# Kernel tuning notes

Measured on AMD Instinct MI355X. Metric: run time of the kernel, lower is better.

## Reference

```python
import jax, jax.numpy as jnp
import numpy as np

N_NODES = 100000
N_EDGES = 1600000
D = 128
NEG_SLOPE = 0.01  # torch F.leaky_relu default


def setup_inputs() -> dict:
    key = jax.random.key(0)
    k1, k2, k3, k4, k5 = jax.random.split(key, 5)
    nfeat = jax.random.normal(k1, (N_NODES, D), dtype=jnp.float32)
    edge_src = jax.random.randint(k2, (N_EDGES,), 0, N_NODES, dtype=jnp.int32)
    edge_dst = jax.random.randint(k3, (N_EDGES,), 0, N_NODES, dtype=jnp.int32)
    edge_w = jax.random.uniform(k4, (N_EDGES,), dtype=jnp.float32)
    W = jax.random.normal(k5, (D, D), dtype=jnp.float32) * (1.0 / np.sqrt(D))
    return {"nfeat": nfeat, "edge_src": edge_src, "edge_dst": edge_dst,
            "edge_w": edge_w, "W": W}


def reference(nfeat, edge_src, edge_dst, edge_w, W):
    # message: m_e = h[src_e] * w_e  (u_mul_e)
    msg = nfeat[edge_src] * edge_w[:, None]          # [E, D]
    # reduce: h_neighbor[v] = sum_{e: dst(e)=v} m_e  (fn.sum)
    h_neighbor = jax.ops.segment_sum(msg, edge_dst, num_segments=nfeat.shape[0])  # [N, D]
    # Bi-interaction residual: leaky_relu(Linear(h * h_neighbor)); dropout = identity (eval)
    out = jax.nn.leaky_relu((nfeat * h_neighbor) @ W.T, negative_slope=NEG_SLOPE)
    return out
```

## Files before the change

kernel.cpp:

```cpp
#include <hip/hip_runtime.h>
#include <hip/hip_fp16.h>

#define NNODES 100000
#define NEDGES 1600000
#define DIM    128
#define NEG_SLOPE 0.01f
#define NB_SCAN ((NNODES + 1023) / 1024)
#define NPART 8
#define PART_SZ ((NNODES + NPART - 1) / NPART)
#define PCAP 220000
#define PCUR_STRIDE 32
#define CHUNK 2048
#define GEMM_TILES ((NNODES + 63) / 64)

typedef _Float16     v8h __attribute__((ext_vector_type(8)));
typedef float        v4f __attribute__((ext_vector_type(4)));
typedef int          v4i __attribute__((ext_vector_type(4)));
typedef int          v2i __attribute__((ext_vector_type(2)));
typedef float        v4x __attribute__((ext_vector_type(4)));
typedef unsigned int v2u __attribute__((ext_vector_type(2)));
typedef unsigned int v4u __attribute__((ext_vector_type(4)));

static inline size_t align256(size_t x) { return (x + 255) & ~(size_t)255; }

union HU { unsigned int u; __half2 h; };

__global__ __launch_bounds__(256) void zero_f32(float* __restrict__ p, int n4) {
    int i = blockIdx.x * blockDim.x + threadIdx.x;
    int stride = gridDim.x * blockDim.x;
    float4 z = make_float4(0.f, 0.f, 0.f, 0.f);
    for (; i < n4; i += stride) ((float4*)p)[i] = z;
}

__global__ __launch_bounds__(256) void prep(const float* __restrict__ nf,
                                            __half* __restrict__ nf16,
                                            int* __restrict__ counts,
                                            int* __restrict__ pcur) {
    int i = blockIdx.x * 256 + threadIdx.x;
    int stride = gridDim.x * 256;
    for (int j = i; j < NNODES * DIM / 4; j += stride) {
        v4x v = __builtin_nontemporal_load((const v4x*)nf + j);
        HU a, b;
        a.h = __float22half2_rn(make_float2(v.x, v.y));
        b.h = __float22half2_rn(make_float2(v.z, v.w));
        ((uint2*)nf16)[j] = make_uint2(a.u, b.u);
    }
    v4i z = (v4i){0, 0, 0, 0};
    for (int j = i; j < NNODES / 4; j += stride)
        *((v4i*)counts + j) = z;
    if (i < NPART * PCUR_STRIDE) pcur[i] = 0;
}

__global__ __launch_bounds__(256) void split_edges(const int* __restrict__ esrc,
                                                   const int* __restrict__ edst,
                                                   const float* __restrict__ ew,
                                                   int* __restrict__ pcur,
                                                   int2* __restrict__ pairs) {
    __shared__ int wtot[4][NPART];
    __shared__ int wbase[4][NPART];
    __shared__ int gbase[NPART];
    int tid = threadIdx.x;
    int wave = tid >> 6, lane = tid & 63;
    unsigned long long lt = (1ull << lane) - 1ull;

    int nq = NEDGES / 4;
    int qA = (blockIdx.x * CHUNK >> 2) + tid;
    int qB = qA + 256;

    v4i dA = (v4i){0,0,0,0}, sA = (v4i){0,0,0,0};
    v4x wA = (v4x){0,0,0,0};
    v4i dB = (v4i){0,0,0,0}, sB = (v4i){0,0,0,0};
    v4x wB = (v4x){0,0,0,0};
    bool vA = qA < nq, vB = qB < nq;
    if (vA) {
        dA = __builtin_nontemporal_load((const v4i*)edst + qA);
        sA = __builtin_nontemporal_load((const v4i*)esrc + qA);
        wA = __builtin_nontemporal_load((const v4x*)ew + qA);
    }
    if (vB) {
        dB = __builtin_nontemporal_load((const v4i*)edst + qB);
        sB = __builtin_nontemporal_load((const v4i*)esrc + qB);
        wB = __builtin_nontemporal_load((const v4x*)ew + qB);
    }

    int prt[8]; int rnk[8]; int2 pv[8];
    #pragma unroll
    for (int k = 0; k < 4; ++k) {
        int d = dA[k], s = sA[k];
        int p = vA ? (int)((unsigned)d / PART_SZ) : -1;
        prt[k] = p;
        pv[k] = make_int2(((d - p * PART_SZ) << 17) | s, __float_as_int(wA[k]));
        int d2 = dB[k], s2 = sB[k];
        int p2 = vB ? (int)((unsigned)d2 / PART_SZ) : -1;
        prt[k + 4] = p2;
        pv[k + 4] = make_int2(((d2 - p2 * PART_SZ) << 17) | s2, __float_as_int(wB[k]));
    }

    int runcnt = 0;
    #pragma unroll
    for (int s = 0; s < 8; ++s) {
        int myp = prt[s];
        unsigned long long mymask = 0;
        int addc = 0;
        #pragma unroll
        for (int p = 0; p < NPART; ++p) {
            unsigned long long m = __ballot(myp == p);
            if (myp == p) mymask = m;
            if (lane == p) addc = (int)__popcll(m);
        }
        int wr = __shfl(runcnt, myp < 0 ? 0 : myp);
        rnk[s] = wr + (int)__popcll(mymask & lt);
        runcnt += addc;
    }

    if (lane < NPART) wtot[wave][lane] = runcnt;
    __syncthreads();
    if (tid < NPART) {
        int t0 = wtot[0][tid], t1 = wtot[1][tid], t2 = wtot[2][tid], t3 = wtot[3][tid];
        wbase[0][tid] = 0; wbase[1][tid] = t0;
        wbase[2][tid] = t0 + t1; wbase[3][tid] = t0 + t1 + t2;
        gbase[tid] = atomicAdd(&pcur[tid * PCUR_STRIDE], t0 + t1 + t2 + t3);
    }
    __syncthreads();

    #pragma unroll
    for (int s = 0; s < 8; ++s) {
        int p = prt[s];
        if (p >= 0) {
            int slot = gbase[p] + wbase[wave][p] + rnk[s];
            if (slot < PCAP)
                pairs[(size_t)p * PCAP + slot] = pv[s];
        }
    }
}

__global__ __launch_bounds__(256) void hist_part(const int2* __restrict__ pairs,
                                                 const int* __restrict__ pcur,
                                                 int* __restrict__ counts) {
    int part = blockIdx.x & (NPART - 1);
    int n = pcur[part * PCUR_STRIDE];
    if (n > PCAP) n = PCAP;
    const int2* base = pairs + (size_t)part * PCAP;
    int cbase = part * PART_SZ;
    int t = (blockIdx.x >> 3) * 256 + threadIdx.x;
    int stride = (gridDim.x >> 3) * 256;
    for (int i = t; i < n; i += stride) {
        int2 pr = base[i];
        atomicAdd(&counts[cbase + ((unsigned)pr.x >> 17)], 1);
    }
}

__global__ __launch_bounds__(256) void scan1(const int* __restrict__ counts,
                                             int* __restrict__ offsets,
                                             int* __restrict__ blocksum) {
    __shared__ int lds[256];
    int tid = threadIdx.x;
    int base = blockIdx.x * 1024 + tid * 4;
    int c0 = (base + 0 < NNODES) ? counts[base + 0] : 0;
    int c1 = (base + 1 < NNODES) ? counts[base + 1] : 0;
    int c2 = (base + 2 < NNODES) ? counts[base + 2] : 0;
    int c3 = (base + 3 < NNODES) ? counts[base + 3] : 0;
    int t = c0 + c1 + c2 + c3;
    lds[tid] = t;
    __syncthreads();
    for (int d = 1; d < 256; d <<= 1) {
        int v = lds[tid];
        int add = (tid >= d) ? lds[tid - d] : 0;
        __syncthreads();
        lds[tid] = v + add;
        __syncthreads();
    }
    int incl = lds[tid];
    int excl = incl - t;
    if (base + 0 < NNODES) offsets[base + 0] = excl;
    if (base + 1 < NNODES) offsets[base + 1] = excl + c0;
    if (base + 2 < NNODES) offsets[base + 2] = excl + c0 + c1;
    if (base + 3 < NNODES) offsets[base + 3] = excl + c0 + c1 + c2;
    if (tid == 255) blocksum[blockIdx.x] = incl;
}

__global__ __launch_bounds__(128) void scan2p(int* __restrict__ blocksum, int nb) {
    __shared__ int lds[128];
    int tid = threadIdx.x;
    int v = (tid < nb) ? blocksum[tid] : 0;
    lds[tid] = v;
    __syncthreads();
    for (int d = 1; d < 128; d <<= 1) {
        int x = lds[tid];
        int add = (tid >= d) ? lds[tid - d] : 0;
        __syncthreads();
        lds[tid] = x + add;
        __syncthreads();
    }
    if (tid < nb) blocksum[tid] = lds[tid] - v;
}

__global__ __launch_bounds__(256) void scan3(int* __restrict__ offsets,
                                             const int* __restrict__ blocksum,
                                             int* __restrict__ cursor) {
    int add = blocksum[blockIdx.x];
    int base = blockIdx.x * 1024 + threadIdx.x * 4;
    #pragma unroll
    for (int i = 0; i < 4; ++i) {
        int idx = base + i;
        if (idx < NNODES) { int o = offsets[idx] + add; offsets[idx] = o; cursor[idx] = o; }
    }
}

__global__ __launch_bounds__(256) void fill_part2(const int2* __restrict__ pairs,
                                                  const int* __restrict__ pcur,
                                                  int* __restrict__ cursor,
                                                  int2* __restrict__ bins) {
    int part = blockIdx.x & (NPART - 1);
    int n = pcur[part * PCUR_STRIDE];
    if (n > PCAP) n = PCAP;
    const int2* base = pairs + (size_t)part * PCAP;
    int cbase = part * PART_SZ;
    int t = (blockIdx.x >> 3) * 256 + threadIdx.x;
    int stride = (gridDim.x >> 3) * 256;
    for (int i = t; i < n; i += stride) {
        int2 pr = base[i];
        int d = cbase + ((unsigned)pr.x >> 17);
        int p = atomicAdd(&cursor[d], 1);
        bins[p] = make_int2(pr.x & 0x1FFFF, pr.y);
    }
}

__global__ __launch_bounds__(256) void pull_x16(const __half* __restrict__ nf16,
                                                const int* __restrict__ offsets,
                                                const int* __restrict__ counts,
                                                const int2* __restrict__ bins,
                                                __half* __restrict__ x16) {
    int gid = blockIdx.x * 256 + threadIdx.x;
    int v = gid >> 5;
    int lane = gid & 31;
    if (v >= NNODES) return;
    int start = offsets[v];
    int end = start + counts[v];
    const uint2* nf2 = (const uint2*)nf16;
    float4 a0 = make_float4(0.f, 0.f, 0.f, 0.f);
    float4 a1 = make_float4(0.f, 0.f, 0.f, 0.f);
    float4 a2 = make_float4(0.f, 0.f, 0.f, 0.f);
    float4 a3 = make_float4(0.f, 0.f, 0.f, 0.f);
    int k = start;
    for (; k + 4 <= end; k += 4) {
        v2i e0 = __builtin_nontemporal_load((const v2i*)bins + k);
        v2i e1 = __builtin_nontemporal_load((const v2i*)bins + k + 1);
        v2i e2 = __builtin_nontemporal_load((const v2i*)bins + k + 2);
        v2i e3 = __builtin_nontemporal_load((const v2i*)bins + k + 3);
        uint2 u0 = nf2[(size_t)e0.x * 32 + lane];
        uint2 u1 = nf2[(size_t)e1.x * 32 + lane];
        uint2 u2 = nf2[(size_t)e2.x * 32 + lane];
        uint2 u3 = nf2[(size_t)e3.x * 32 + lane];
        float w0 = __int_as_float(e0.y), w1 = __int_as_float(e1.y);
        float w2 = __int_as_float(e2.y), w3 = __int_as_float(e3.y);
        HU h; float2 f;
        h.u = u0.x; f = __half22float2(h.h); a0.x += w0 * f.x; a0.y += w0 * f.y;
        h.u = u0.y; f = __half22float2(h.h); a0.z += w0 * f.x; a0.w += w0 * f.y;
        h.u = u1.x; f = __half22float2(h.h); a1.x += w1 * f.x; a1.y += w1 * f.y;
        h.u = u1.y; f = __half22float2(h.h); a1.z += w1 * f.x; a1.w += w1 * f.y;
        h.u = u2.x; f = __half22float2(h.h); a2.x += w2 * f.x; a2.y += w2 * f.y;
        h.u = u2.y; f = __half22float2(h.h); a2.z += w2 * f.x; a2.w += w2 * f.y;
        h.u = u3.x; f = __half22float2(h.h); a3.x += w3 * f.x; a3.y += w3 * f.y;
        h.u = u3.y; f = __half22float2(h.h); a3.z += w3 * f.x; a3.w += w3 * f.y;
    }
    for (; k < end; ++k) {
        v2i e = __builtin_nontemporal_load((const v2i*)bins + k);
        float w = __int_as_float(e.y);
        uint2 u = nf2[(size_t)e.x * 32 + lane];
        HU h; float2 f;
        h.u = u.x; f = __half22float2(h.h); a0.x += w * f.x; a0.y += w * f.y;
        h.u = u.y; f = __half22float2(h.h); a0.z += w * f.x; a0.w += w * f.y;
    }
    float4 acc;
    acc.x = (a0.x + a1.x) + (a2.x + a3.x);
    acc.y = (a0.y + a1.y) + (a2.y + a3.y);
    acc.z = (a0.z + a1.z) + (a2.z + a3.z);
    acc.w = (a0.w + a1.w) + (a2.w + a3.w);
    uint2 un = nf2[(size_t)v * 32 + lane];
    HU h; float2 f;
    h.u = un.x; f = __half22float2(h.h); acc.x *= f.x; acc.y *= f.y;
    h.u = un.y; f = __half22float2(h.h); acc.z *= f.x; acc.w *= f.y;
    HU o0, o1;
    o0.h = __float22half2_rn(make_float2(acc.x, acc.y));
    o1.h = __float22half2_rn(make_float2(acc.z, acc.w));
    v2u ov = (v2u){o0.u, o1.u};
    __builtin_nontemporal_store(ov, (v2u*)x16 + (size_t)v * 32 + lane);
}

__global__ __launch_bounds__(256) void gemm16(const __half* __restrict__ x16,
                                              const float* __restrict__ W,
                                              float* __restrict__ out) {
    __shared__ _Float16 Wl[128 * 128];
    __shared__ _Float16 Xl[64 * 128];
    int tid = threadIdx.x;

    const float4* Wg = (const float4*)W;
    for (int i = tid; i < 2048; i += 256) {
        int r = i >> 4, c = i & 15;
        float4 lo = Wg[(r * 128 + c * 8) >> 2];
        float4 hi = Wg[((r * 128 + c * 8) >> 2) + 1];
        v8h h;
        h[0] = (_Float16)lo.x; h[1] = (_Float16)lo.y; h[2] = (_Float16)lo.z; h[3] = (_Float16)lo.w;
        h[4] = (_Float16)hi.x; h[5] = (_Float16)hi.y; h[6] = (_Float16)hi.z; h[7] = (_Float16)hi.w;
        *(v8h*)&Wl[r * 128 + (c ^ (r & 7)) * 8] = h;
    }

    int rbase = blockIdx.x * 64;
    for (int i = tid; i < 1024; i += 256) {
        int r = i >> 4, c = i & 15;
        int grow = rbase + r;
        v4u u = (v4u){0u, 0u, 0u, 0u};
        if (grow < NNODES)
            u = __builtin_nontemporal_load((const v4u*)x16 + (size_t)grow * 16 + c);
        *(v4u*)&Xl[r * 128 + (c ^ (r & 7)) * 8] = u;
    }
    __syncthreads();

    int wave = tid >> 6;
    int lane = tid & 63;
    int n = lane & 15;
    int g = lane >> 4;

    v4f acc[8];
    #pragma unroll
    for (int jb = 0; jb < 8; ++jb) acc[jb] = (v4f){0.f, 0.f, 0.f, 0.f};

    #pragma unroll
    for (int kb = 0; kb < 4; ++kb) {
        v8h a = *(v8h*)&Xl[(wave * 16 + n) * 128 + (((kb * 4 + g) ^ (n & 7)) * 8)];
        #pragma unroll
        for (int jb = 0; jb < 8; ++jb) {
            v8h b = *(v8h*)&Wl[(jb * 16 + n) * 128 + (((kb * 4 + g) ^ (n & 7)) * 8)];
            acc[jb] = __builtin_amdgcn_mfma_f32_16x16x32_f16(a, b, acc[jb], 0, 0, 0);
        }
    }

    int row0 = rbase + wave * 16 + g * 4;
    #pragma unroll
    for (int jb = 0; jb < 8; ++jb) {
        #pragma unroll
        for (int reg = 0; reg < 4; ++reg) {
            int r = row0 + reg;
            if (r < NNODES) {
                float v = acc[jb][reg];
                v = v >= 0.f ? v : NEG_SLOPE * v;
                __builtin_nontemporal_store(v, out + (size_t)r * 128 + jb * 16 + n);
            }
        }
    }
}

__global__ __launch_bounds__(256) void hist_dst4(const int* __restrict__ edst,
                                                 int* __restrict__ counts) {
    int i = blockIdx.x * 256 + threadIdx.x;
    if (i < NEDGES / 4) {
        int4 d = ((const int4*)edst)[i];
        atomicAdd(&counts[d.x], 1);
        atomicAdd(&counts[d.y], 1);
        atomicAdd(&counts[d.z], 1);
        atomicAdd(&counts[d.w], 1);
    }
}

__global__ __launch_bounds__(256) void fill_part(const int* __restrict__ esrc,
                                                 const int* __restrict__ edst,
                                                 const float* __restrict__ ew,
                                                 int* __restrict__ cursor,
                                                 int2* __restrict__ bins) {
    int part = blockIdx.x & (NPART - 1);
    int lo = part * PART_SZ;
    int hi = lo + PART_SZ;
    int t = (blockIdx.x >> 3) * 256 + threadIdx.x;
    int stride = (gridDim.x >> 3) * 256;
    int nq = NEDGES / 4;
    for (int i = t; i < nq; i += stride) {
        int4 d = ((const int4*)edst)[i];
        int e = i * 4;
        if (d.x >= lo && d.x < hi) {
            int p = atomicAdd(&cursor[d.x], 1);
            bins[p] = make_int2(esrc[e + 0], __float_as_int(ew[e + 0]));
        }
        if (d.y >= lo && d.y < hi) {
            int p = atomicAdd(&cursor[d.y], 1);
            bins[p] = make_int2(esrc[e + 1], __float_as_int(ew[e + 1]));
        }
        if (d.z >= lo && d.z < hi) {
            int p = atomicAdd(&cursor[d.z], 1);
            bins[p] = make_int2(esrc[e + 2], __float_as_int(ew[e + 2]));
        }
        if (d.w >= lo && d.w < hi) {
            int p = atomicAdd(&cursor[d.w], 1);
            bins[p] = make_int2(esrc[e + 3], __float_as_int(ew[e + 3]));
        }
    }
}

__global__ __launch_bounds__(256) void scatter_edges(
    const float* __restrict__ nfeat, const int* __restrict__ esrc,
    const int* __restrict__ edst, const float* __restrict__ ew,
    float* __restrict__ hn) {
    long long t = (long long)blockIdx.x * 256 + threadIdx.x;
    int e = (int)(t >> 5);
    if (e >= NEDGES) return;
    int lane = (int)(t & 31);
    int s = esrc[e];
    int d = edst[e];
    float w = ew[e];
    float4 v = ((const float4*)(nfeat + (size_t)s * DIM))[lane];
    float* o = hn + (size_t)d * DIM + lane * 4;
    unsafeAtomicAdd(o + 0, v.x * w);
    unsafeAtomicAdd(o + 1, v.y * w);
    unsafeAtomicAdd(o + 2, v.z * w);
    unsafeAtomicAdd(o + 3, v.w * w);
}

__global__ __launch_bounds__(256) void elem_mul(const float* __restrict__ nfeat,
                                                float* __restrict__ hn, int n4) {
    int i = blockIdx.x * blockDim.x + threadIdx.x;
    int stride = gridDim.x * blockDim.x;
    for (; i < n4; i += stride) {
        float4 a = ((const float4*)nfeat)[i];
        float4 b = ((float4*)hn)[i];
        b.x *= a.x; b.y *= a.y; b.z *= a.z; b.w *= a.w;
        ((float4*)hn)[i] = b;
    }
}

__global__ __launch_bounds__(256) void bi_gemm2(
    const float* __restrict__ x, const float* __restrict__ W,
    float* __restrict__ out) {
    extern __shared__ float lds[];
    float4* W4  = (float4*)lds;
    float*  xs  = lds + 128 * 128;
    float4* xs4 = (float4*)xs;
    int tid = threadIdx.x;
    const float4* Wg = (const float4*)W;
    for (int i = tid; i < 128 * 32; i += 256) {
        int j = i >> 5, d4 = i & 31;
        W4[(j << 5) | (d4 ^ ((j >> 2) & 7))] = Wg[i];
    }
    __syncthreads();
    int tx = tid & 31, ty = tid >> 5;
    int j0 = tx << 2, r0 = ty << 2;
    int ntiles = NNODES / 32;
    for (int tile = blockIdx.x; tile < ntiles; tile += gridDim.x) {
        int rbase = tile * 32;
        for (int i = tid; i < 32 * 32; i += 256)
            xs4[i] = ((const float4*)x)[(size_t)rbase * 32 + i];
        __syncthreads();
        float acc[4][4];
        #pragma unroll
        for (int r = 0; r < 4; ++r)
            #pragma unroll
            for (int j = 0; j < 4; ++j) acc[r][j] = 0.f;
        #pragma unroll 4
        for (int d4 = 0; d4 < 32; ++d4) {
            float4 xv[4], wv[4];
            #pragma unroll
            for (int r = 0; r < 4; ++r) xv[r] = xs4[((r0 + r) << 5) | d4];
            #pragma unroll
            for (int j = 0; j < 4; ++j) {
                int jj = j0 + j;
                wv[j] = W4[(jj << 5) | (d4 ^ ((jj >> 2) & 7))];
            }
            #pragma unroll
            for (int r = 0; r < 4; ++r)
                #pragma unroll
                for (int j = 0; j < 4; ++j) {
                    acc[r][j] += xv[r].x * wv[j].x;
                    acc[r][j] += xv[r].y * wv[j].y;
                    acc[r][j] += xv[r].z * wv[j].z;
                    acc[r][j] += xv[r].w * wv[j].w;
                }
        }
        __syncthreads();
        #pragma unroll
        for (int r = 0; r < 4; ++r) {
            float4 o;
            o.x = acc[r][0] >= 0.f ? acc[r][0] : NEG_SLOPE * acc[r][0];
            o.y = acc[r][1] >= 0.f ? acc[r][1] : NEG_SLOPE * acc[r][1];
            o.z = acc[r][2] >= 0.f ? acc[r][2] : NEG_SLOPE * acc[r][2];
            o.w = acc[r][3] >= 0.f ? acc[r][3] : NEG_SLOPE * acc[r][3];
            size_t row = (size_t)(rbase + r0 + r);
            ((float4*)out)[row * (DIM / 4) + tx] = o;
        }
    }
}

extern "C" void kernel_launch(void* const* d_in, const int* in_sizes, int n_in,
                              void* d_out, int out_size, void* d_ws, size_t ws_size,
                              hipStream_t stream) {
    const float* nfeat = (const float*)d_in[0];
    const int*   esrc  = (const int*)d_in[1];
    const int*   edst  = (const int*)d_in[2];
    const float* ew    = (const float*)d_in[3];
    const float* W     = (const float*)d_in[4];
    float* out = (float*)d_out;

    size_t off = 0;
    size_t nf16_off = off;     off += align256((size_t)NNODES * DIM * 2);
    size_t x16_off = off;      off += align256((size_t)NNODES * DIM * 2);
    size_t cnt_off = off;      off += align256((size_t)NNODES * 4);
    size_t ofs_off = off;      off += align256((size_t)NNODES * 4);
    size_t cur_off = off;      off += align256((size_t)NNODES * 4);
    size_t pcur_off = off;     off += align256((size_t)NPART * PCUR_STRIDE * 4);
    size_t bsum_off = off;     off += align256((size_t)NB_SCAN * 4);
    size_t bins_off = off;     off += align256((size_t)NEDGES * 8);
    size_t need_mid = off;
    size_t pair_off = off;     off += align256((size_t)NPART * PCAP * 8);
    size_t need_full = off;

    char* ws = (char*)d_ws;

    if (ws_size >= need_mid) {
        __half* nf16 = (__half*)(ws + nf16_off);
        __half* x16  = (__half*)(ws + x16_off);
        int* counts = (int*)(ws + cnt_off);
        int* offsets = (int*)(ws + ofs_off);
        int* cursor = (int*)(ws + cur_off);
        int* pcur = (int*)(ws + pcur_off);
        int* blocksum = (int*)(ws + bsum_off);
        int2* bins = (int2*)(ws + bins_off);
        int2* pairs = (int2*)(ws + pair_off);

        prep<<<2048, 256, 0, stream>>>(nfeat, nf16, counts, pcur);
        if (ws_size >= need_full) {
            int sgrid = (NEDGES + CHUNK - 1) / CHUNK;
            split_edges<<<sgrid, 256, 0, stream>>>(esrc, edst, ew, pcur, pairs);
            hist_part<<<2048, 256, 0, stream>>>(pairs, pcur, counts);
            scan1<<<NB_SCAN, 256, 0, stream>>>(counts, offsets, blocksum);
            scan2p<<<1, 128, 0, stream>>>(blocksum, NB_SCAN);
            scan3<<<NB_SCAN, 256, 0, stream>>>(offsets, blocksum, cursor);
            fill_part2<<<2048, 256, 0, stream>>>(pairs, pcur, cursor, bins);
        } else {
            int e4grid = (NEDGES / 4 + 255) / 256;
            hist_dst4<<<e4grid, 256, 0, stream>>>(edst, counts);
            scan1<<<NB_SCAN, 256, 0, stream>>>(counts, offsets, blocksum);
            scan2p<<<1, 128, 0, stream>>>(blocksum, NB_SCAN);
            scan3<<<NB_SCAN, 256, 0, stream>>>(offsets, blocksum, cursor);
            fill_part<<<2048, 256, 0, stream>>>(esrc, edst, ew, cursor, bins);
        }
        int pgrid = (NNODES * 32 + 255) / 256;
        pull_x16<<<pgrid, 256, 0, stream>>>(nf16, offsets, counts, bins, x16);
        gemm16<<<GEMM_TILES, 256, 0, stream>>>(x16, W, out);
    } else {
        float* hn = (float*)ws;
        hipFuncSetAttribute((const void*)bi_gemm2,
                            hipFuncAttributeMaxDynamicSharedMemorySize, 81920);
        zero_f32<<<2048, 256, 0, stream>>>(hn, NNODES * DIM / 4);
        int sgrid = (NEDGES * 32 + 255) / 256;
        scatter_edges<<<sgrid, 256, 0, stream>>>(nfeat, esrc, edst, ew, hn);
        elem_mul<<<2048, 256, 0, stream>>>(nfeat, hn, NNODES * DIM / 4);
        bi_gemm2<<<512, 256, 81920, stream>>>(hn, W, out);
    }
}
```

Before: 274.6 us.

## Fuse neighbor pull into GEMM kernel with fp16 accumulation and prepacked W

```diff
diff --git a/kernel.cpp b/kernel.cpp
--- a/kernel.cpp
+++ b/kernel.cpp
@@ -18,12 +18,11 @@
 typedef int          v4i __attribute__((ext_vector_type(4)));
 typedef int          v2i __attribute__((ext_vector_type(2)));
 typedef float        v4x __attribute__((ext_vector_type(4)));
-typedef unsigned int v2u __attribute__((ext_vector_type(2)));
-typedef unsigned int v4u __attribute__((ext_vector_type(4)));
 
 static inline size_t align256(size_t x) { return (x + 255) & ~(size_t)255; }
 
 union HU { unsigned int u; __half2 h; };
+union U4H { uint4 u; __half2 h[4]; };
 
 __global__ __launch_bounds__(256) void zero_f32(float* __restrict__ p, int n4) {
     int i = blockIdx.x * blockDim.x + threadIdx.x;
@@ -33,7 +32,9 @@
 }
 
 __global__ __launch_bounds__(256) void prep(const float* __restrict__ nf,
+                                            const float* __restrict__ W,
                                             __half* __restrict__ nf16,
+                                            __half* __restrict__ W16,
                                             int* __restrict__ counts,
                                             int* __restrict__ pcur) {
     int i = blockIdx.x * 256 + threadIdx.x;
@@ -44,6 +45,16 @@
         a.h = __float22half2_rn(make_float2(v.x, v.y));
         b.h = __float22half2_rn(make_float2(v.z, v.w));
         ((uint2*)nf16)[j] = make_uint2(a.u, b.u);
+    }
+    const float4* Wg4 = (const float4*)W;
+    for (int j = i; j < DIM * DIM / 8; j += stride) {
+        float4 lo = Wg4[j * 2], hi = Wg4[j * 2 + 1];
+        HU a, b, c, d;
+        a.h = __float22half2_rn(make_float2(lo.x, lo.y));
+        b.h = __float22half2_rn(make_float2(lo.z, lo.w));
+        c.h = __float22half2_rn(make_float2(hi.x, hi.y));
+        d.h = __float22half2_rn(make_float2(hi.z, hi.w));
+        ((uint4*)W16)[j] = make_uint4(a.u, b.u, c.u, d.u);
     }
     v4i z = (v4i){0, 0, 0, 0};
     for (int j = i; j < NNODES / 4; j += stride)
@@ -144,8 +155,14 @@
     int cbase = part * PART_SZ;
     int t = (blockIdx.x >> 3) * 256 + threadIdx.x;
     int stride = (gridDim.x >> 3) * 256;
-    for (int i = t; i < n; i += stride) {
-        int2 pr = base[i];
+    int nh = n >> 1;
+    for (int i = t; i < nh; i += stride) {
+        v4i pr = __builtin_nontemporal_load((const v4i*)base + i);
+        atomicAdd(&counts[cbase + ((unsigned)pr.x >> 17)], 1);
+        atomicAdd(&counts[cbase + ((unsigned)pr.z >> 17)], 1);
+    }
+    if ((blockIdx.x >> 3) == 0 && threadIdx.x == 0 && (n & 1)) {
+        int2 pr = base[n - 1];
         atomicAdd(&counts[cbase + ((unsigned)pr.x >> 17)], 1);
     }
 }
@@ -196,20 +213,19 @@
 }
 
 __global__ __launch_bounds__(256) void scan3(int* __restrict__ offsets,
-                                             const int* __restrict__ blocksum,
-                                             int* __restrict__ cursor) {
+                                             const int* __restrict__ blocksum) {
     int add = blocksum[blockIdx.x];
     int base = blockIdx.x * 1024 + threadIdx.x * 4;
     #pragma unroll
     for (int i = 0; i < 4; ++i) {
         int idx = base + i;
-        if (idx < NNODES) { int o = offsets[idx] + add; offsets[idx] = o; cursor[idx] = o; }
+        if (idx < NNODES) offsets[idx] += add;
     }
 }
 
 __global__ __launch_bounds__(256) void fill_part2(const int2* __restrict__ pairs,
                                                   const int* __restrict__ pcur,
-                                                  int* __restrict__ cursor,
+                                                  int* __restrict__ offsets,
                                                   int2* __restrict__ bins) {
     int part = blockIdx.x & (NPART - 1);
     int n = pcur[part * PCUR_STRIDE];
@@ -218,102 +234,87 @@
     int cbase = part * PART_SZ;
     int t = (blockIdx.x >> 3) * 256 + threadIdx.x;
     int stride = (gridDim.x >> 3) * 256;
-    for (int i = t; i < n; i += stride) {
-        int2 pr = base[i];
+    int nh = n >> 1;
+    for (int i = t; i < nh; i += stride) {
+        v4i pr = __builtin_nontemporal_load((const v4i*)base + i);
+        int d0 = cbase + ((unsigned)pr.x >> 17);
+        int p0 = atomicAdd(&offsets[d0], 1);
+        bins[p0] = make_int2(pr.x & 0x1FFFF, pr.y);
+        int d1 = cbase + ((unsigned)pr.z >> 17);
+        int p1 = atomicAdd(&offsets[d1], 1);
+        bins[p1] = make_int2(pr.z & 0x1FFFF, pr.w);
+    }
+    if ((blockIdx.x >> 3) == 0 && threadIdx.x == 0 && (n & 1)) {
+        int2 pr = base[n - 1];
         int d = cbase + ((unsigned)pr.x >> 17);
-        int p = atomicAdd(&cursor[d], 1);
+        int p = atomicAdd(&offsets[d], 1);
         bins[p] = make_int2(pr.x & 0x1FFFF, pr.y);
     }
 }
 
-__global__ __launch_bounds__(256) void pull_x16(const __half* __restrict__ nf16,
-                                                const int* __restrict__ offsets,
-                                                const int* __restrict__ counts,
-                                                const int2* __restrict__ bins,
-                                                __half* __restrict__ x16) {
-    int gid = blockIdx.x * 256 + threadIdx.x;
-    int v = gid >> 5;
-    int lane = gid & 31;
-    if (v >= NNODES) return;
-    int start = offsets[v];
-    int end = start + counts[v];
-    const uint2* nf2 = (const uint2*)nf16;
-    float4 a0 = make_float4(0.f, 0.f, 0.f, 0.f);
-    float4 a1 = make_float4(0.f, 0.f, 0.f, 0.f);
-    float4 a2 = make_float4(0.f, 0.f, 0.f, 0.f);
-    float4 a3 = make_float4(0.f, 0.f, 0.f, 0.f);
-    int k = start;
-    for (; k + 4 <= end; k += 4) {
-        v2i e0 = __builtin_nontemporal_load((const v2i*)bins + k);
-        v2i e1 = __builtin_nontemporal_load((const v2i*)bins + k + 1);
-        v2i e2 = __builtin_nontemporal_load((const v2i*)bins + k + 2);
-        v2i e3 = __builtin_nontemporal_load((const v2i*)bins + k + 3);
-        uint2 u0 = nf2[(size_t)e0.x * 32 + lane];
-        uint2 u1 = nf2[(size_t)e1.x * 32 + lane];
-        uint2 u2 = nf2[(size_t)e2.x * 32 + lane];
-        uint2 u3 = nf2[(size_t)e3.x * 32 + lane];
-        float w0 = __int_as_float(e0.y), w1 = __int_as_float(e1.y);
-        float w2 = __int_as_float(e2.y), w3 = __int_as_float(e3.y);
-        HU h; float2 f;
-        h.u = u0.x; f = __half22float2(h.h); a0.x += w0 * f.x; a0.y += w0 * f.y;
-        h.u = u0.y; f = __half22float2(h.h); a0.z += w0 * f.x; a0.w += w0 * f.y;
-        h.u = u1.x; f = __half22float2(h.h); a1.x += w1 * f.x; a1.y += w1 * f.y;
-        h.u = u1.y; f = __half22float2(h.h); a1.z += w1 * f.x; a1.w += w1 * f.y;
-        h.u = u2.x; f = __half22float2(h.h); a2.x += w2 * f.x; a2.y += w2 * f.y;
-        h.u = u2.y; f = __half22float2(h.h); a2.z += w2 * f.x; a2.w += w2 * f.y;
-        h.u = u3.x; f = __half22float2(h.h); a3.x += w3 * f.x; a3.y += w3 * f.y;
-        h.u = u3.y; f = __half22float2(h.h); a3.z += w3 * f.x; a3.w += w3 * f.y;
-    }
-    for (; k < end; ++k) {
-        v2i e = __builtin_nontemporal_load((const v2i*)bins + k);
-        float w = __int_as_float(e.y);
-        uint2 u = nf2[(size_t)e.x * 32 + lane];
-        HU h; float2 f;
-        h.u = u.x; f = __half22float2(h.h); a0.x += w * f.x; a0.y += w * f.y;
-        h.u = u.y; f = __half22float2(h.h); a0.z += w * f.x; a0.w += w * f.y;
-    }
-    float4 acc;
-    acc.x = (a0.x + a1.x) + (a2.x + a3.x);
-    acc.y = (a0.y + a1.y) + (a2.y + a3.y);
-    acc.z = (a0.z + a1.z) + (a2.z + a3.z);
-    acc.w = (a0.w + a1.w) + (a2.w + a3.w);
-    uint2 un = nf2[(size_t)v * 32 + lane];
-    HU h; float2 f;
-    h.u = un.x; f = __half22float2(h.h); acc.x *= f.x; acc.y *= f.y;
-    h.u = un.y; f = __half22float2(h.h); acc.z *= f.x; acc.w *= f.y;
-    HU o0, o1;
-    o0.h = __float22half2_rn(make_float2(acc.x, acc.y));
-    o1.h = __float22half2_rn(make_float2(acc.z, acc.w));
-    v2u ov = (v2u){o0.u, o1.u};
-    __builtin_nontemporal_store(ov, (v2u*)x16 + (size_t)v * 32 + lane);
-}
-
-__global__ __launch_bounds__(256) void gemm16(const __half* __restrict__ x16,
-                                              const float* __restrict__ W,
-                                              float* __restrict__ out) {
-    __shared__ _Float16 Wl[128 * 128];
+__global__ __launch_bounds__(256) void pull_gemm(const __half* __restrict__ nf16,
+                                                 const __half* __restrict__ W16,
+                                                 const int* __restrict__ offsets,
+                                                 const int* __restrict__ counts,
+                                                 const int2* __restrict__ bins,
+                                                 float* __restrict__ out) {
     __shared__ _Float16 Xl[64 * 128];
     int tid = threadIdx.x;
-
-    const float4* Wg = (const float4*)W;
-    for (int i = tid; i < 2048; i += 256) {
-        int r = i >> 4, c = i & 15;
-        float4 lo = Wg[(r * 128 + c * 8) >> 2];
-        float4 hi = Wg[((r * 128 + c * 8) >> 2) + 1];
-        v8h h;
-        h[0] = (_Float16)lo.x; h[1] = (_Float16)lo.y; h[2] = (_Float16)lo.z; h[3] = (_Float16)lo.w;
-        h[4] = (_Float16)hi.x; h[5] = (_Float16)hi.y; h[6] = (_Float16)hi.z; h[7] = (_Float16)hi.w;
-        *(v8h*)&Wl[r * 128 + (c ^ (r & 7)) * 8] = h;
-    }
-
     int rbase = blockIdx.x * 64;
-    for (int i = tid; i < 1024; i += 256) {
-        int r = i >> 4, c = i & 15;
-        int grow = rbase + r;
-        v4u u = (v4u){0u, 0u, 0u, 0u};
-        if (grow < NNODES)
-            u = __builtin_nontemporal_load((const v4u*)x16 + (size_t)grow * 16 + c);
-        *(v4u*)&Xl[r * 128 + (c ^ (r & 7)) * 8] = u;
+    int gg = tid >> 4;
+    int l  = tid & 15;
+    const uint4* nfu4 = (const uint4*)nf16;
+
+    #pragma unroll
+    for (int t = 0; t < 4; ++t) {
+        int r = gg * 4 + t;
+        int v = rbase + r;
+        if (v < NNODES) {
+            int end = offsets[v];
+            int start = end - counts[v];
+            __half2 z2 = __float2half2_rn(0.f);
+            U4H a0, a1, a2, a3;
+            #pragma unroll
+            for (int j = 0; j < 4; ++j) { a0.h[j] = z2; a1.h[j] = z2; a2.h[j] = z2; a3.h[j] = z2; }
+            int k = start;
+            for (; k + 4 <= end; k += 4) {
+                v2i e0 = __builtin_nontemporal_load((const v2i*)bins + k);
+                v2i e1 = __builtin_nontemporal_load((const v2i*)bins + k + 1);
+                v2i e2 = __builtin_nontemporal_load((const v2i*)bins + k + 2);
+                v2i e3 = __builtin_nontemporal_load((const v2i*)bins + k + 3);
+                U4H u0, u1, u2, u3;
+                u0.u = nfu4[(size_t)e0.x * 16 + l];
+                u1.u = nfu4[(size_t)e1.x * 16 + l];
+                u2.u = nfu4[(size_t)e2.x * 16 + l];
+                u3.u = nfu4[(size_t)e3.x * 16 + l];
+                __half2 w0 = __float2half2_rn(__int_as_float(e0.y));
+                __half2 w1 = __float2half2_rn(__int_as_float(e1.y));
+                __half2 w2 = __float2half2_rn(__int_as_float(e2.y));
+                __half2 w3 = __float2half2_rn(__int_as_float(e3.y));
+                #pragma unroll
+                for (int j = 0; j < 4; ++j) {
+                    a0.h[j] = __hfma2(w0, u0.h[j], a0.h[j]);
+                    a1.h[j] = __hfma2(w1, u1.h[j], a1.h[j]);
+                    a2.h[j] = __hfma2(w2, u2.h[j], a2.h[j]);
+                    a3.h[j] = __hfma2(w3, u3.h[j], a3.h[j]);
+                }
+            }
+            for (; k < end; ++k) {
+                v2i e = __builtin_nontemporal_load((const v2i*)bins + k);
+                U4H u; u.u = nfu4[(size_t)e.x * 16 + l];
+                __half2 w = __float2half2_rn(__int_as_float(e.y));
+                #pragma unroll
+                for (int j = 0; j < 4; ++j) a0.h[j] = __hfma2(w, u.h[j], a0.h[j]);
+            }
+            U4H s, sf;
+            sf.u = nfu4[(size_t)v * 16 + l];
+            #pragma unroll
+            for (int j = 0; j < 4; ++j) {
+                __half2 t2 = __hadd2(__hadd2(a0.h[j], a1.h[j]), __hadd2(a2.h[j], a3.h[j]));
+                s.h[j] = __hmul2(t2, sf.h[j]);
+            }
+            *(uint4*)&Xl[r * 128 + ((l ^ (r & 7)) << 3)] = s.u;
+        }
     }
     __syncthreads();
 
@@ -321,6 +322,7 @@
     int lane = tid & 63;
     int n = lane & 15;
     int g = lane >> 4;
+    const v8h* w8 = (const v8h*)W16;
 
     v4f acc[8];
     #pragma unroll
@@ -328,10 +330,10 @@
 
     #pragma unroll
     for (int kb = 0; kb < 4; ++kb) {
-        v8h a = *(v8h*)&Xl[(wave * 16 + n) * 128 + (((kb * 4 + g) ^ (n & 7)) * 8)];
+        v8h a = *(v8h*)&Xl[(wave * 16 + n) * 128 + (((kb * 4 + g) ^ (n & 7)) << 3)];
         #pragma unroll
         for (int jb = 0; jb < 8; ++jb) {
-            v8h b = *(v8h*)&Wl[(jb * 16 + n) * 128 + (((kb * 4 + g) ^ (n & 7)) * 8)];
+            v8h b = w8[(jb * 16 + n) * 16 + kb * 4 + g];
             acc[jb] = __builtin_amdgcn_mfma_f32_16x16x32_f16(a, b, acc[jb], 0, 0, 0);
         }
     }
@@ -366,7 +368,7 @@
 __global__ __launch_bounds__(256) void fill_part(const int* __restrict__ esrc,
                                                  const int* __restrict__ edst,
                                                  const float* __restrict__ ew,
-                                                 int* __restrict__ cursor,
+                                                 int* __restrict__ offsets,
                                                  int2* __restrict__ bins) {
     int part = blockIdx.x & (NPART - 1);
     int lo = part * PART_SZ;
@@ -378,19 +380,19 @@
         int4 d = ((const int4*)edst)[i];
         int e = i * 4;
         if (d.x >= lo && d.x < hi) {
-            int p = atomicAdd(&cursor[d.x], 1);
+            int p = atomicAdd(&offsets[d.x], 1);
             bins[p] = make_int2(esrc[e + 0], __float_as_int(ew[e + 0]));
         }
         if (d.y >= lo && d.y < hi) {
-            int p = atomicAdd(&cursor[d.y], 1);
+            int p = atomicAdd(&offsets[d.y], 1);
             bins[p] = make_int2(esrc[e + 1], __float_as_int(ew[e + 1]));
         }
         if (d.z >= lo && d.z < hi) {
-            int p = atomicAdd(&cursor[d.z], 1);
+            int p = atomicAdd(&offsets[d.z], 1);
             bins[p] = make_int2(esrc[e + 2], __float_as_int(ew[e + 2]));
         }
         if (d.w >= lo && d.w < hi) {
-            int p = atomicAdd(&cursor[d.w], 1);
+            int p = atomicAdd(&offsets[d.w], 1);
             bins[p] = make_int2(esrc[e + 3], __float_as_int(ew[e + 3]));
         }
     }
@@ -500,10 +502,9 @@
 
     size_t off = 0;
     size_t nf16_off = off;     off += align256((size_t)NNODES * DIM * 2);
-    size_t x16_off = off;      off += align256((size_t)NNODES * DIM * 2);
+    size_t w16_off = off;      off += align256((size_t)DIM * DIM * 2);
     size_t cnt_off = off;      off += align256((size_t)NNODES * 4);
     size_t ofs_off = off;      off += align256((size_t)NNODES * 4);
-    size_t cur_off = off;      off += align256((size_t)NNODES * 4);
     size_t pcur_off = off;     off += align256((size_t)NPART * PCUR_STRIDE * 4);
     size_t bsum_off = off;     off += align256((size_t)NB_SCAN * 4);
     size_t bins_off = off;     off += align256((size_t)NEDGES * 8);
@@ -515,35 +516,32 @@
 
     if (ws_size >= need_mid) {
         __half* nf16 = (__half*)(ws + nf16_off);
-        __half* x16  = (__half*)(ws + x16_off);
+        __half* W16  = (__half*)(ws + w16_off);
         int* counts = (int*)(ws + cnt_off);
         int* offsets = (int*)(ws + ofs_off);
-        int* cursor = (int*)(ws + cur_off);
         int* pcur = (int*)(ws + pcur_off);
         int* blocksum = (int*)(ws + bsum_off);
         int2* bins = (int2*)(ws + bins_off);
         int2* pairs = (int2*)(ws + pair_off);
 
-        prep<<<2048, 256, 0, stream>>>(nfeat, nf16, counts, pcur);
+        prep<<<2048, 256, 0, stream>>>(nfeat, W, nf16, W16, counts, pcur);
         if (ws_size >= need_full) {
             int sgrid = (NEDGES + CHUNK - 1) / CHUNK;
             split_edges<<<sgrid, 256, 0, stream>>>(esrc, edst, ew, pcur, pairs);
             hist_part<<<2048, 256, 0, stream>>>(pairs, pcur, counts);
             scan1<<<NB_SCAN, 256, 0, stream>>>(counts, offsets, blocksum);
             scan2p<<<1, 128, 0, stream>>>(blocksum, NB_SCAN);
-            scan3<<<NB_SCAN, 256, 0, stream>>>(offsets, blocksum, cursor);
-            fill_part2<<<2048, 256, 0, stream>>>(pairs, pcur, cursor, bins);
+            scan3<<<NB_SCAN, 256, 0, stream>>>(offsets, blocksum);
+            fill_part2<<<2048, 256, 0, stream>>>(pairs, pcur, offsets, bins);
         } else {
             int e4grid = (NEDGES / 4 + 255) / 256;
             hist_dst4<<<e4grid, 256, 0, stream>>>(edst, counts);
             scan1<<<NB_SCAN, 256, 0, stream>>>(counts, offsets, blocksum);
             scan2p<<<1, 128, 0, stream>>>(blocksum, NB_SCAN);
-            scan3<<<NB_SCAN, 256, 0, stream>>>(offsets, blocksum, cursor);
-            fill_part<<<2048, 256, 0, stream>>>(esrc, edst, ew, cursor, bins);
-        }
-        int pgrid = (NNODES * 32 + 255) / 256;
-        pull_x16<<<pgrid, 256, 0, stream>>>(nf16, offsets, counts, bins, x16);
-        gemm16<<<GEMM_TILES, 256, 0, stream>>>(x16, W, out);
+            scan3<<<NB_SCAN, 256, 0, stream>>>(offsets, blocksum);
+            fill_part<<<2048, 256, 0, stream>>>(esrc, edst, ew, offsets, bins);
+        }
+        pull_gemm<<<GEMM_TILES, 256, 0, stream>>>(nf16, W16, offsets, counts, bins, out);
     } else {
         float* hn = (float*)ws;
         hipFuncSetAttribute((const void*)bi_gemm2,
```

Result: slower. 286.5 us (+4.3%).
